# Kernel tuning notes

Hardware: AMD Instinct MI355X
Metric: run time of the kernel (lower is better)

Reference implementation:

```python
import jax, jax.numpy as jnp
import numpy as np
from jax import lax

B, N, M, K = 8, 4096, 2048, 64   # graphs, points/graph, fps centers/graph (ratio=0.5), max neighbors
R = 0.5                           # radius
F_IN = 64


def setup_inputs() -> dict:
    key = jax.random.key(0)
    ks = jax.random.split(key, 6)
    x = jax.random.normal(ks[0], (B * N, F_IN), jnp.float32)
    pos = jax.random.normal(ks[1], (B * N, 3), jnp.float32)
    batch = jnp.repeat(jnp.arange(B, dtype=jnp.int32), N)  # sorted graph ids
    def lin_w(k, fi, fo):
        return (jax.random.normal(k, (fi, fo), jnp.float32) / np.sqrt(fi)).astype(jnp.float32)
    w1 = lin_w(ks[2], F_IN + 3, 64); b1 = jnp.zeros((64,), jnp.float32)
    w2 = lin_w(ks[3], 64, 64);       b2 = jnp.zeros((64,), jnp.float32)
    w3 = lin_w(ks[4], 64, 128);      b3 = jnp.zeros((128,), jnp.float32)
    return dict(x=x, pos=pos, batch=batch, w1=w1, b1=b1, w2=w2, b2=b2, w3=w3, b3=b3)


def fps(pos_g, m):
    """Farthest point sampling on one graph [n,3] -> m int32 indices (deterministic start at 0)."""
    n = pos_g.shape[0]
    def step(carry, _):
        mind, last = carry
        d = jnp.sum((pos_g - pos_g[last]) ** 2, axis=-1)
        mind = jnp.minimum(mind, d)
        return (mind, jnp.argmax(mind).astype(jnp.int32)), last
    init = (jnp.full((n,), 1e30, jnp.float32), jnp.int32(0))
    _, idx = lax.scan(step, init, None, length=m)
    return idx


def reference(x, pos, batch, w1, b1, w2, b2, w3, b3):
    # batch is sorted with equal-size graphs -> reshape to [B, N, .]
    pos_b = pos.reshape(B, N, 3)
    x_b = x.reshape(B, N, F_IN)

    # fps per graph (PyG.fps with ratio=0.5)
    cidx = jax.vmap(lambda p: fps(p, M))(pos_b)                 # [B, M]
    bi = jnp.arange(B)[:, None]
    pos_c = pos_b[bi, cidx]                                     # [B, M, 3]

    # radius ball query, capped at K neighbors (take K nearest, mask > R)
    d2 = jnp.sum((pos_c[:, :, None, :] - pos_b[:, None, :, :]) ** 2, axis=-1)  # [B, M, N]
    neg_d2k, nbr = lax.top_k(-d2, K)                            # [B, M, K]
    mask = (-neg_d2k) <= R * R                                  # center itself always valid (d=0)

    # PointConv message: nn(concat[x_j, pos_j - pos_i]), then max-aggregate per center
    bii = jnp.arange(B)[:, None, None]
    x_j = x_b[bii, nbr]                                         # [B, M, K, F_IN]
    rel = pos_b[bii, nbr] - pos_c[:, :, None, :]                # [B, M, K, 3]
    h = jnp.concatenate([x_j, rel], axis=-1)                    # [B, M, K, F_IN+3]
    h = jax.nn.relu(h @ w1 + b1)
    h = jax.nn.relu(h @ w2 + b2)
    h = h @ w3 + b3                                             # [B, M, K, 128]
    h = jnp.where(mask[..., None], h, -jnp.inf)
    out = jnp.max(h, axis=2)                                    # [B, M, 128]

    out_x = out.reshape(B * M, 128)
    out_pos = pos_c.reshape(B * M, 3)
    out_batch = jnp.repeat(jnp.arange(B, dtype=jnp.int32), M)
    return out_x, out_pos, out_batch
```

## Files before the change

### kernel.cpp

```cpp
#include <hip/hip_runtime.h>

#define BG 8
#define NP 4096
#define MC 2048
#define KN 64
#define NWK 248
#define CAND 480

__device__ __forceinline__ float dist2(float ax, float ay, float az,
                                       float bx, float by, float bz) {
    float dx = __fsub_rn(ax, bx), dy = __fsub_rn(ay, by), dz = __fsub_rn(az, bz);
    return __fadd_rn(__fadd_rn(__fmul_rn(dx, dx), __fmul_rn(dy, dy)), __fmul_rn(dz, dz));
}

template <int CTRL>
__device__ __forceinline__ float dppmax(float v) {
    int t = __builtin_amdgcn_update_dpp(0, __float_as_int(v), CTRL, 0xf, 0xf, true);
    return fmaxf(v, __int_as_float(t));
}

__global__ __launch_bounds__(512, 1) void k_fused(
    const float* __restrict__ pos, const float* __restrict__ x,
    const float* __restrict__ w1, const float* __restrict__ b1,
    const float* __restrict__ w2, const float* __restrict__ b2,
    const float* __restrict__ w3, const float* __restrict__ b3,
    float* __restrict__ y,
    float* __restrict__ out_pos, float* __restrict__ out_batch, float* __restrict__ out_x,
    int* __restrict__ prog, int* __restrict__ yready)
{
    __shared__ float smem[24576];
    const int tid = threadIdx.x;
    if (blockIdx.x < BG) {
        const int b = blockIdx.x;
        const float* pg = pos + (size_t)b * NP * 3;
        for (int i = tid; i < NP * 3; i += 512) smem[i] = pg[i];
        __syncthreads();
        const int lane = tid & 63, wv = tid >> 6;
        float px[8], py[8], pz[8], mind[8];
        const int base = tid * 8;
        #pragma unroll
        for (int i = 0; i < 8; i++) {
            px[i] = smem[(base + i) * 3];
            py[i] = smem[(base + i) * 3 + 1];
            pz[i] = smem[(base + i) * 3 + 2];
            mind[i] = 1e30f;
        }
        float2* sl = (float2*)(smem + NP * 3);
        float cx = smem[0], cy = smem[1], cz = smem[2];
        if (tid == 0) {
            const size_t c3 = (size_t)b * MC * 3;
            __hip_atomic_store(&out_pos[c3 + 0], cx, __ATOMIC_RELAXED, __HIP_MEMORY_SCOPE_AGENT);
            __hip_atomic_store(&out_pos[c3 + 1], cy, __ATOMIC_RELAXED, __HIP_MEMORY_SCOPE_AGENT);
            __hip_atomic_store(&out_pos[c3 + 2], cz, __ATOMIC_RELAXED, __HIP_MEMORY_SCOPE_AGENT);
        }
        for (int m = 1; m < MC; m++) {
            float bv = -1.0f; int bi = base;
            #pragma unroll
            for (int i = 0; i < 8; i++) {
                float d = dist2(px[i], py[i], pz[i], cx, cy, cz);
                float nm = fminf(mind[i], d);
                mind[i] = nm;
                if (nm > bv) { bv = nm; bi = base + i; }
            }
            float v = bv;
            v = dppmax<0x111>(v);
            v = dppmax<0x112>(v);
            v = dppmax<0x114>(v);
            v = dppmax<0x118>(v);
            v = dppmax<0x142>(v);
            v = dppmax<0x143>(v);
            const float V = __int_as_float(__builtin_amdgcn_readlane(__float_as_int(v), 63));
            unsigned long long mk = __ballot(bv == V);
            float2* sb = sl + (m & 1) * 8;
            if (lane == (int)(__ffsll((long long)mk) - 1))
                sb[wv] = make_float2(V, __int_as_float(bi));
            __syncthreads();
            const float4* sq = (const float4*)sb;
            float4 q0 = sq[0], q1 = sq[1], q2 = sq[2], q3 = sq[3];
            float Vg = q0.x; int ig = __float_as_int(q0.y);
            if (q0.z > Vg) { Vg = q0.z; ig = __float_as_int(q0.w); }
            if (q1.x > Vg) { Vg = q1.x; ig = __float_as_int(q1.y); }
            if (q1.z > Vg) { Vg = q1.z; ig = __float_as_int(q1.w); }
            if (q2.x > Vg) { Vg = q2.x; ig = __float_as_int(q2.y); }
            if (q2.z > Vg) { Vg = q2.z; ig = __float_as_int(q2.w); }
            if (q3.x > Vg) { Vg = q3.x; ig = __float_as_int(q3.y); }
            if (q3.z > Vg) { Vg = q3.z; ig = __float_as_int(q3.w); }
            cx = smem[ig * 3]; cy = smem[ig * 3 + 1]; cz = smem[ig * 3 + 2];
            if (tid == 0) {
                const size_t c3 = (size_t)(b * MC + m) * 3;
                __hip_atomic_store(&out_pos[c3 + 0], cx, __ATOMIC_RELAXED, __HIP_MEMORY_SCOPE_AGENT);
                __hip_atomic_store(&out_pos[c3 + 1], cy, __ATOMIC_RELAXED, __HIP_MEMORY_SCOPE_AGENT);
                __hip_atomic_store(&out_pos[c3 + 2], cz, __ATOMIC_RELAXED, __HIP_MEMORY_SCOPE_AGENT);
                __hip_atomic_store(&prog[b * 16], m, __ATOMIC_RELAXED, __HIP_MEMORY_SCOPE_AGENT);
            }
        }
        __syncthreads();
        if (tid == 0)
            __hip_atomic_store(&prog[b * 16], MC, __ATOMIC_RELEASE, __HIP_MEMORY_SCOPE_AGENT);
        for (int i = tid; i < MC; i += 512) out_batch[b * MC + i] = (float)b;
    } else {
        const int w = blockIdx.x - BG;
        const int g = w & 7;
        const int sub = w >> 3;
        const int lane = tid & 63, ww = tid >> 6;
        const int waveid = sub * 8 + ww;
        float* wsm = smem;
        for (int i = tid; i < 4096; i += 512) wsm[i] = w1[i];
        const float b1v = b1[lane];
        __syncthreads();
        const int p0 = sub * 133;
        const int p1 = (p0 + 133 < NP) ? p0 + 133 : NP;
        const float* xg = x + (size_t)g * NP * 64;
        float* yg_w = y + (size_t)g * NP * 64;
        for (int p = p0 + ww; p < p1; p += 8) {
            float xrow = xg[(size_t)p * 64 + lane];
            float acc = b1v;
            #pragma unroll
            for (int f = 0; f < 64; f++) {
                float xf = __shfl(xrow, f, 64);
                acc = fmaf(xf, wsm[f * 64 + lane], acc);
            }
            yg_w[(size_t)p * 64 + lane] = acc;
        }
        __syncthreads();
        if (tid == 0)
            __hip_atomic_fetch_add(&yready[g * 16], 1, __ATOMIC_RELEASE, __HIP_MEMORY_SCOPE_AGENT);
        float w2c[64], w3a[64], w3b[64];
        #pragma unroll
        for (int f = 0; f < 64; f++) {
            w2c[f] = w2[f * 64 + lane];
            w3a[f] = w3[f * 128 + lane];
            w3b[f] = w3[f * 128 + 64 + lane];
        }
        const float b2v = b2[lane], b3av = b3[lane], b3bv = b3[lane + 64];
        const float wp0 = w1[64 * 64 + lane], wp1 = w1[65 * 64 + lane], wp2 = w1[66 * 64 + lane];
        while (__hip_atomic_load(&yready[g * 16], __ATOMIC_RELAXED, __HIP_MEMORY_SCOPE_AGENT) < 31)
            __builtin_amdgcn_s_sleep(16);
        {
            int yr = __hip_atomic_load(&yready[g * 16], __ATOMIC_ACQUIRE, __HIP_MEMORY_SCOPE_AGENT);
            asm volatile("" :: "v"(yr));
        }
        float2* cand = (float2*)(smem + 4096) + ww * CAND;
        int* nlist = (int*)(smem + 11776) + ww * 64;
        float* st1 = smem + 12288 + ww * 136;
        float* st2 = st1 + 68;
        const float* pg = pos + (size_t)g * NP * 3;
        const float* yg = y + (size_t)g * NP * 64;
        for (int m = waveid; m < MC; m += NWK) {
            int cur;
            while ((cur = __hip_atomic_load(&prog[g * 16], __ATOMIC_RELAXED, __HIP_MEMORY_SCOPE_AGENT)) <= m) {
                if (m - cur > 16) __builtin_amdgcn_s_sleep(64);
                else              __builtin_amdgcn_s_sleep(8);
            }
            const int ci = g * MC + m;
            const size_t c3 = (size_t)ci * 3;
            const float cx = __hip_atomic_load(&out_pos[c3 + 0], __ATOMIC_RELAXED, __HIP_MEMORY_SCOPE_AGENT);
            const float cy = __hip_atomic_load(&out_pos[c3 + 1], __ATOMIC_RELAXED, __HIP_MEMORY_SCOPE_AGENT);
            const float cz = __hip_atomic_load(&out_pos[c3 + 2], __ATOMIC_RELAXED, __HIP_MEMORY_SCOPE_AGENT);
            int cnt = 0;
            for (int c = 0; c < 64; c++) {
                const int p = c * 64 + lane;
                float ppx = pg[p * 3], ppy = pg[p * 3 + 1], ppz = pg[p * 3 + 2];
                float d2 = dist2(ppx, ppy, ppz, cx, cy, cz);
                bool inr = d2 <= 0.25f;
                unsigned long long mk = __ballot(inr);
                int pre = __popcll(mk & ((1ull << lane) - 1ull));
                int wp = cnt + pre;
                if (inr && wp < CAND) cand[wp] = make_float2(d2, __int_as_float(p));
                cnt += __popcll(mk);
            }
            if (cnt > CAND) cnt = CAND;
            int kc;
            if (cnt <= KN) {
                kc = cnt;
                if (lane < cnt) nlist[lane] = __float_as_int(cand[lane].y);
            } else {
                kc = KN;
                for (int basej = 0; basej < cnt; basej += 64) {
                    int jj = basej + lane;
                    float dj = 3.4e38f; int ij = 0x7fffffff;
                    bool act = jj < cnt;
                    if (act) { float2 e = cand[jj]; dj = e.x; ij = __float_as_int(e.y); }
                    int rank = 0;
                    for (int l = 0; l < cnt; l++) {
                        float2 e = cand[l];
                        float dl = e.x; int il = __float_as_int(e.y);
                        if (dl < dj || (dl == dj && il < ij)) rank++;
                    }
                    if (act && rank < KN) nlist[rank] = ij;
                }
            }
            float mA = -3.4e38f, mB = -3.4e38f;
            for (int k = 0; k < kc; k++) {
                const int j = nlist[k];
                const float yv = yg[(size_t)j * 64 + lane];
                const float jx = pg[j * 3], jy = pg[j * 3 + 1], jz = pg[j * 3 + 2];
                float rx = jx - cx, ry = jy - cy, rz = jz - cz;
                float h1 = fmaf(rx, wp0, yv);
                h1 = fmaf(ry, wp1, h1);
                h1 = fmaf(rz, wp2, h1);
                h1 = fmaxf(h1, 0.f);
                st1[lane] = h1;
                float a2a = b2v, a2b = 0.f;
                #pragma unroll
                for (int fc = 0; fc < 16; fc += 2) {
                    float4 hA = *(const float4*)&st1[fc * 4];
                    float4 hB = *(const float4*)&st1[fc * 4 + 4];
                    a2a = fmaf(hA.x, w2c[fc * 4], a2a);
                    a2a = fmaf(hA.y, w2c[fc * 4 + 1], a2a);
                    a2a = fmaf(hA.z, w2c[fc * 4 + 2], a2a);
                    a2a = fmaf(hA.w, w2c[fc * 4 + 3], a2a);
                    a2b = fmaf(hB.x, w2c[fc * 4 + 4], a2b);
                    a2b = fmaf(hB.y, w2c[fc * 4 + 5], a2b);
                    a2b = fmaf(hB.z, w2c[fc * 4 + 6], a2b);
                    a2b = fmaf(hB.w, w2c[fc * 4 + 7], a2b);
                }
                float h2 = fmaxf(a2a + a2b, 0.f);
                st2[lane] = h2;
                float a3 = b3av, a4 = b3bv;
                #pragma unroll
                for (int fc = 0; fc < 16; fc++) {
                    float4 h = *(const float4*)&st2[fc * 4];
                    a3 = fmaf(h.x, w3a[fc * 4], a3);
                    a3 = fmaf(h.y, w3a[fc * 4 + 1], a3);
                    a3 = fmaf(h.z, w3a[fc * 4 + 2], a3);
                    a3 = fmaf(h.w, w3a[fc * 4 + 3], a3);
                    a4 = fmaf(h.x, w3b[fc * 4], a4);
                    a4 = fmaf(h.y, w3b[fc * 4 + 1], a4);
                    a4 = fmaf(h.z, w3b[fc * 4 + 2], a4);
                    a4 = fmaf(h.w, w3b[fc * 4 + 3], a4);
                }
                mA = fmaxf(mA, a3);
                mB = fmaxf(mB, a4);
            }
            out_x[(size_t)ci * 128 + lane] = mA;
            out_x[(size_t)ci * 128 + 64 + lane] = mB;
        }
    }
}

extern "C" void kernel_launch(void* const* d_in, const int* in_sizes, int n_in,
                              void* d_out, int out_size, void* d_ws, size_t ws_size,
                              hipStream_t stream) {
    const float* x   = (const float*)d_in[0];
    const float* pos = (const float*)d_in[1];
    const float* w1  = (const float*)d_in[3];
    const float* b1  = (const float*)d_in[4];
    const float* w2  = (const float*)d_in[5];
    const float* b2  = (const float*)d_in[6];
    const float* w3  = (const float*)d_in[7];
    const float* b3  = (const float*)d_in[8];

    float* out_x     = (float*)d_out;
    float* out_pos   = out_x + (size_t)BG * MC * 128;
    float* out_batch = out_pos + (size_t)BG * MC * 3;

    char* ws    = (char*)d_ws;
    float* y    = (float*)ws;
    int* prog   = (int*)(ws + 8388608);
    int* yready = (int*)(ws + 8389120);

    (void)hipMemsetAsync(prog, 0, 1024, stream);
    hipLaunchKernelGGL(k_fused, dim3(256), dim3(512), 0, stream,
                       pos, x, w1, b1, w2, b2, w3, b3,
                       y, out_pos, out_batch, out_x, prog, yready);
}
```

Before: 1.363 ms.

## Pack two FPS graphs per block with per-graph LDS atomic barriers

The FPS phase now runs two graphs in one 512-thread block. Each graph gets four waves, and each thread handles 16 points instead of 8. The block-wide __syncthreads per iteration is replaced by a per-graph atomic counter barrier in LDS with spin-wait, so the two graphs progress independently and the cross-wave reduction only spans 4 entries. This frees four blocks for the downstream workers, but it doubles per-thread serial work in the FPS loop and adds spin-barrier overhead. The worker-block index and grid size are adjusted to match.

After: 1.903 ms. 39.6% more time.

```diff
diff --git a/kernel.cpp b/kernel.cpp
--- a/kernel.cpp
+++ b/kernel.cpp
@@ -28,26 +28,34 @@
     float* __restrict__ out_pos, float* __restrict__ out_batch, float* __restrict__ out_x,
     int* __restrict__ prog, int* __restrict__ yready)
 {
-    __shared__ float smem[24576];
+    __shared__ float smem[24640];
     const int tid = threadIdx.x;
-    if (blockIdx.x < BG) {
-        const int b = blockIdx.x;
-        const float* pg = pos + (size_t)b * NP * 3;
-        for (int i = tid; i < NP * 3; i += 512) smem[i] = pg[i];
+    if (blockIdx.x < 4) {
+        const int blk = blockIdx.x;
+        const int lane = tid & 63, wv = tid >> 6;
+        const int g = wv >> 2, wq = wv & 3;
+        const int b = blk * 2 + g;
+        float* posL = smem + g * 12288;
+        int* bar = (int*)(smem + 24576) + g * 16;
+        float2* sl = (float2*)(smem + 24608) + g * 8;
+        {
+            const float* src = pos + (size_t)blk * 2 * NP * 3;
+            for (int i = tid; i < 2 * NP * 3; i += 512) smem[i] = src[i];
+        }
+        if (tid < 32) ((int*)(smem + 24576))[tid] = 0;
         __syncthreads();
-        const int lane = tid & 63, wv = tid >> 6;
-        float px[8], py[8], pz[8], mind[8];
-        const int base = tid * 8;
+        const int tgrp = wq * 64 + lane;
+        float px[16], py[16], pz[16], mind[16];
+        const int base = tgrp * 16;
         #pragma unroll
-        for (int i = 0; i < 8; i++) {
-            px[i] = smem[(base + i) * 3];
-            py[i] = smem[(base + i) * 3 + 1];
-            pz[i] = smem[(base + i) * 3 + 2];
+        for (int i = 0; i < 16; i++) {
+            px[i] = posL[(base + i) * 3];
+            py[i] = posL[(base + i) * 3 + 1];
+            pz[i] = posL[(base + i) * 3 + 2];
             mind[i] = 1e30f;
         }
-        float2* sl = (float2*)(smem + NP * 3);
-        float cx = smem[0], cy = smem[1], cz = smem[2];
-        if (tid == 0) {
+        float cx = posL[0], cy = posL[1], cz = posL[2];
+        if (tgrp == 0) {
             const size_t c3 = (size_t)b * MC * 3;
             __hip_atomic_store(&out_pos[c3 + 0], cx, __ATOMIC_RELAXED, __HIP_MEMORY_SCOPE_AGENT);
             __hip_atomic_store(&out_pos[c3 + 1], cy, __ATOMIC_RELAXED, __HIP_MEMORY_SCOPE_AGENT);
@@ -56,7 +64,7 @@
         for (int m = 1; m < MC; m++) {
             float bv = -1.0f; int bi = base;
             #pragma unroll
-            for (int i = 0; i < 8; i++) {
+            for (int i = 0; i < 16; i++) {
                 float d = dist2(px[i], py[i], pz[i], cx, cy, cz);
                 float nm = fminf(mind[i], d);
                 mind[i] = nm;
@@ -71,22 +79,23 @@
             v = dppmax<0x143>(v);
             const float V = __int_as_float(__builtin_amdgcn_readlane(__float_as_int(v), 63));
             unsigned long long mk = __ballot(bv == V);
-            float2* sb = sl + (m & 1) * 8;
+            float2* sb = sl + (m & 1) * 4;
             if (lane == (int)(__ffsll((long long)mk) - 1))
-                sb[wv] = make_float2(V, __int_as_float(bi));
-            __syncthreads();
+                sb[wq] = make_float2(V, __int_as_float(bi));
+            if (lane == 0)
+                __hip_atomic_fetch_add(bar, 1, __ATOMIC_RELEASE, __HIP_MEMORY_SCOPE_WORKGROUP);
+            const int target = 4 * m;
+            while (__hip_atomic_load(bar, __ATOMIC_ACQUIRE, __HIP_MEMORY_SCOPE_WORKGROUP) < target)
+                __builtin_amdgcn_s_sleep(1);
             const float4* sq = (const float4*)sb;
-            float4 q0 = sq[0], q1 = sq[1], q2 = sq[2], q3 = sq[3];
+            float4 q0 = sq[0], q1 = sq[1];
             float Vg = q0.x; int ig = __float_as_int(q0.y);
             if (q0.z > Vg) { Vg = q0.z; ig = __float_as_int(q0.w); }
             if (q1.x > Vg) { Vg = q1.x; ig = __float_as_int(q1.y); }
             if (q1.z > Vg) { Vg = q1.z; ig = __float_as_int(q1.w); }
-            if (q2.x > Vg) { Vg = q2.x; ig = __float_as_int(q2.y); }
-            if (q2.z > Vg) { Vg = q2.z; ig = __float_as_int(q2.w); }
-            if (q3.x > Vg) { Vg = q3.x; ig = __float_as_int(q3.y); }
-            if (q3.z > Vg) { Vg = q3.z; ig = __float_as_int(q3.w); }
-            cx = smem[ig * 3]; cy = smem[ig * 3 + 1]; cz = smem[ig * 3 + 2];
-            if (tid == 0) {
+            cx = posL[ig * 3]; cy = posL[ig * 3 + 1]; cz = posL[ig * 3 + 2];
+            if (tgrp == 0) {
+                asm volatile("s_waitcnt vmcnt(0)" ::: "memory");
                 const size_t c3 = (size_t)(b * MC + m) * 3;
                 __hip_atomic_store(&out_pos[c3 + 0], cx, __ATOMIC_RELAXED, __HIP_MEMORY_SCOPE_AGENT);
                 __hip_atomic_store(&out_pos[c3 + 1], cy, __ATOMIC_RELAXED, __HIP_MEMORY_SCOPE_AGENT);
@@ -94,12 +103,13 @@
                 __hip_atomic_store(&prog[b * 16], m, __ATOMIC_RELAXED, __HIP_MEMORY_SCOPE_AGENT);
             }
         }
-        __syncthreads();
-        if (tid == 0)
+        if (tgrp == 0) {
+            asm volatile("s_waitcnt vmcnt(0)" ::: "memory");
             __hip_atomic_store(&prog[b * 16], MC, __ATOMIC_RELEASE, __HIP_MEMORY_SCOPE_AGENT);
-        for (int i = tid; i < MC; i += 512) out_batch[b * MC + i] = (float)b;
+        }
+        for (int i = tgrp; i < MC; i += 256) out_batch[b * MC + i] = (float)b;
     } else {
-        const int w = blockIdx.x - BG;
+        const int w = blockIdx.x - 4;
         const int g = w & 7;
         const int sub = w >> 3;
         const int lane = tid & 63, ww = tid >> 6;
@@ -261,7 +271,7 @@
     int* yready = (int*)(ws + 8389120);
 
     (void)hipMemsetAsync(prog, 0, 1024, stream);
-    hipLaunchKernelGGL(k_fused, dim3(256), dim3(512), 0, stream,
+    hipLaunchKernelGGL(k_fused, dim3(252), dim3(512), 0, stream,
                        pos, x, w1, b1, w2, b2, w3, b3,
                        y, out_pos, out_batch, out_x, prog, yready);
 }
```
